# Kernel optimization log

Measured on AMD Instinct MI355X. Metric: run time of the kernel, lower is better.

Reference implementation:

```python
import jax, jax.numpy as jnp
import numpy as np

N = 100000      # nodes
E = 1600000     # edges (avg degree 16)
D_IN, D_HID, D_OUT = 128, 64, 32


def setup_inputs() -> dict:
    key = jax.random.key(0)
    ks = jax.random.split(key, 11)
    g = lambda k, shape, fan: jax.random.normal(k, shape, jnp.float32) * (1.0 / np.sqrt(fan))
    return {
        "x": jax.random.normal(ks[0], (N, D_IN), jnp.float32),
        "edges_index": jax.random.randint(ks[1], (2, E), 0, N, dtype=jnp.int64),
        # GATConv layer 1 (heads=1): linear weight, attention vectors a_src/a_dst, bias
        "W1": g(ks[2], (D_IN, D_HID), D_IN),
        "a_src1": g(ks[3], (D_HID,), D_HID),
        "a_dst1": g(ks[4], (D_HID,), D_HID),
        "b1": jnp.zeros((D_HID,), jnp.float32),
        # GATConv layer 2
        "W2": g(ks[5], (D_HID, D_OUT), D_HID),
        "a_src2": g(ks[6], (D_OUT,), D_OUT),
        "a_dst2": g(ks[7], (D_OUT,), D_OUT),
        "b2": jnp.zeros((D_OUT,), jnp.float32),
    }


def _gat_conv(x, src, dst, W, a_src, a_dst, b, n):
    """Single-head PyG GATConv: transform, edge attention, per-dst softmax, scatter-add."""
    h = x @ W                                        # [N, D]
    e = jax.nn.leaky_relu((h @ a_src)[src] + (h @ a_dst)[dst], 0.2)  # [E']
    # segment softmax over edges grouped by destination node
    m = jax.ops.segment_max(e, dst, num_segments=n)  # [N]
    w = jnp.exp(e - m[dst])                          # [E']
    s = jax.ops.segment_sum(w, dst, num_segments=n)  # [N]
    att = w / (s[dst] + 1e-16)                       # [E']
    out = jax.ops.segment_sum(att[:, None] * h[src], dst, num_segments=n)  # [N, D]
    return out + b


def reference(x, edges_index, W1, a_src1, a_dst1, b1, W2, a_src2, a_dst2, b2):
    n = x.shape[0]
    loops = jnp.arange(n, dtype=edges_index.dtype)   # GATConv add_self_loops=True
    src = jnp.concatenate([edges_index[0], loops])
    dst = jnp.concatenate([edges_index[1], loops])
    h = jax.nn.relu(_gat_conv(x, src, dst, W1, a_src1, a_dst1, b1, n))
    # F.dropout with training=False is identity (eval mode)
    out = _gat_conv(h, src, dst, W2, a_src2, a_dst2, b2, n)
    return jax.nn.log_softmax(out, axis=1)
```

## Files before the change

kernel.cpp:

```cpp
#include <hip/hip_runtime.h>
#include <math.h>

#define D_IN 128
#define D_HID 64
#define D_OUT 32
#define CAP 48
#define BSH 8
#define NB 391
#define CAPB 4608
#define CHUNK 8192
#define NPW 4
#define ESHIFT 5.0f
#define ECLAMP 16.0f

typedef __fp16 half2f __attribute__((ext_vector_type(2)));

__device__ __forceinline__ half2f u2h2(unsigned u) {
    union { unsigned u; half2f h; } c; c.u = u; return c.h;
}
__device__ __forceinline__ unsigned h22u(half2f h) {
    union { half2f h; unsigned u; } c; c.h = h; return c.u;
}
__device__ __forceinline__ unsigned short f2h(float f) {
    union { _Float16 h; unsigned short u; } c; c.h = (_Float16)f; return c.u;
}

#if defined(__has_builtin)
#  if __has_builtin(__builtin_amdgcn_fdot2)
#    define HAVE_FDOT2 1
#  else
#    define HAVE_FDOT2 0
#  endif
#else
#  define HAVE_FDOT2 0
#endif

__device__ __forceinline__ float fdot2f(half2f a, half2f b, float c) {
#if HAVE_FDOT2
    return __builtin_amdgcn_fdot2(a, b, c, false);
#else
    return fmaf((float)a.y, (float)b.y, fmaf((float)a.x, (float)b.x, c));
#endif
}

__device__ __forceinline__ void pair_acc(float wA, float wB, uint2 hA, uint2 hB,
                                         float& a0, float& a1, float& a2, float& a3)
{
    half2f wp = __builtin_amdgcn_cvt_pkrtz(wA, wB);
    a0 = fdot2f(wp, u2h2(__builtin_amdgcn_perm(hB.x, hA.x, 0x05040100u)), a0);
    a1 = fdot2f(wp, u2h2(__builtin_amdgcn_perm(hB.x, hA.x, 0x07060302u)), a1);
    a2 = fdot2f(wp, u2h2(__builtin_amdgcn_perm(hB.y, hA.y, 0x05040100u)), a2);
    a3 = fdot2f(wp, u2h2(__builtin_amdgcn_perm(hB.y, hA.y, 0x07060302u)), a3);
}


__global__ __launch_bounds__(256) void init_kernel(
    int* __restrict__ cnt, int* __restrict__ cursor, int n)
{
    int i = blockIdx.x * 256 + threadIdx.x;
    if (i < n) cnt[i] = 0;
    if (i < NB) cursor[i] = i * CAPB;
}

__global__ __launch_bounds__(256) void part_kernel(
    const int* __restrict__ esrc, const int* __restrict__ edst,
    unsigned long long* __restrict__ ebuf, int* __restrict__ cursor,
    int E, int Et)
{
    __shared__ int hist[NB];
    __shared__ int ofs[NB];
    const int t = threadIdx.x;
    const int base = blockIdx.x * CHUNK;
    const int end = min(base + CHUNK, Et);

    for (int b = t; b < NB; b += 256) hist[b] = 0;
    __syncthreads();
    for (int i = base + t; i < end; i += 256) {
        int d = (i < E) ? edst[i] : (i - E);
        atomicAdd(&hist[d >> BSH], 1);
    }
    __syncthreads();
    for (int b = t; b < NB; b += 256) {
        int c = hist[b];
        ofs[b] = c ? atomicAdd(&cursor[b], c) : 0;
    }
    __syncthreads();
    for (int i = base + t; i < end; i += 256) {
        int d = (i < E) ? edst[i] : (i - E);
        int s = (i < E) ? esrc[i] : (i - E);
        int p = atomicAdd(&ofs[d >> BSH], 1);
        ebuf[p] = ((unsigned long long)(unsigned)s << 32) | (unsigned)d;
    }
}

__global__ __launch_bounds__(256) void fill_bucket_kernel(
    const unsigned long long* __restrict__ ebuf, const int* __restrict__ cursor,
    int* __restrict__ cnt, int* __restrict__ csr_pad)
{
    int b = blockIdx.x;
    int beg = b * CAPB;
    int end = cursor[b];
    for (int i = beg + threadIdx.x; i < end; i += 256) {
        unsigned long long v = ebuf[i];
        int d = (int)(v & 0xffffffffu);
        int s = (int)(v >> 32);
        int slot = atomicAdd(&cnt[d], 1);
        if (slot < CAP) csr_pad[(size_t)d * CAP + slot] = s;
    }
}


template<int K, int NC, int RT, int PAD>
__global__ __launch_bounds__(256) void gemm_alpha_kernel(
    const float* __restrict__ A, const float* __restrict__ W,
    const float* __restrict__ a_src, const float* __restrict__ a_dst,
    unsigned short* __restrict__ C, float* __restrict__ as_,
    float* __restrict__ ad_, int M)
{
    constexpr int TM = 64;
    constexpr int CT = 4;
    constexpr int CG = NC / CT;
    constexpr int KS = K + PAD;
    __shared__ float xs[TM * KS];
    __shared__ float ws[K * NC];
    const int t = threadIdx.x;

    for (int i = t; i < K * NC / 4; i += 256)
        ((float4*)ws)[i] = ((const float4*)W)[i];

    const int base = blockIdx.x * TM;
    for (int i = t; i < TM * K / 4; i += 256) {
        int nloc = i / (K / 4);
        int k4   = i % (K / 4);
        int row  = base + nloc;
        float4 v = make_float4(0.f, 0.f, 0.f, 0.f);
        if (row < M)
            v = *(const float4*)(A + (size_t)row * K + k4 * 4);
        *(float4*)(xs + nloc * KS + k4 * 4) = v;
    }
    __syncthreads();

    const int tx = t % CG, ty = t / CG;
    const int r0 = ty * RT, c0 = tx * CT;
    float acc[RT][CT];
#pragma unroll
    for (int i = 0; i < RT; ++i)
#pragma unroll
        for (int j = 0; j < CT; ++j) acc[i][j] = 0.f;

    for (int k = 0; k < K; k += 4) {
        float4 a[RT];
#pragma unroll
        for (int i = 0; i < RT; ++i)
            a[i] = *(const float4*)(xs + (r0 + i) * KS + k);
#pragma unroll
        for (int kk = 0; kk < 4; ++kk) {
            float4 b = *(const float4*)(ws + (k + kk) * NC + c0);
#pragma unroll
            for (int i = 0; i < RT; ++i) {
                float av = kk == 0 ? a[i].x : kk == 1 ? a[i].y :
                           kk == 2 ? a[i].z : a[i].w;
                acc[i][0] = fmaf(av, b.x, acc[i][0]);
                acc[i][1] = fmaf(av, b.y, acc[i][1]);
                acc[i][2] = fmaf(av, b.z, acc[i][2]);
                acc[i][3] = fmaf(av, b.w, acc[i][3]);
            }
        }
    }

    const float4 asv = *(const float4*)(a_src + c0);
    const float4 adv = *(const float4*)(a_dst + c0);
#pragma unroll
    for (int i = 0; i < RT; ++i) {
        int row = base + r0 + i;
        float ps = acc[i][0] * asv.x + acc[i][1] * asv.y +
                   acc[i][2] * asv.z + acc[i][3] * asv.w;
        float pd = acc[i][0] * adv.x + acc[i][1] * adv.y +
                   acc[i][2] * adv.z + acc[i][3] * adv.w;
#pragma unroll
        for (int o = 1; o < CG; o <<= 1) {
            ps += __shfl_xor(ps, o);
            pd += __shfl_xor(pd, o);
        }
        if (row < M) {
            uint2 cv;
            cv.x = h22u(__builtin_amdgcn_cvt_pkrtz(acc[i][0], acc[i][1]));
            cv.y = h22u(__builtin_amdgcn_cvt_pkrtz(acc[i][2], acc[i][3]));
            *(uint2*)(C + (size_t)row * NC + c0) = cv;
            if (tx == 0) { as_[row] = ps; ad_[row] = pd; }
        }
    }
}

__global__ __launch_bounds__(256) void gat_aggr_fused_kernel(
    const int* __restrict__ cnt, const int* __restrict__ csr_pad,
    const float* __restrict__ as1, const float* __restrict__ ad1,
    const unsigned short* __restrict__ h1, const float* __restrict__ b1,
    const float* __restrict__ W2, const float* __restrict__ a2s,
    const float* __restrict__ a2d, unsigned short* __restrict__ h2,
    float* __restrict__ as2, float* __restrict__ ad2, int n)
{
    __shared__ float rbuf[4][64];
    const int t = threadIdx.x;
    const int wave = t >> 6;
    const int lane = t & 63;
    const int half = lane >> 5, j = lane & 31;

    float w2r[32];
#pragma unroll
    for (int k = 0; k < 32; ++k)
        w2r[k] = W2[(size_t)(half * 32 + k) * D_OUT + j];
    const float a2sj = a2s[j], a2dj = a2d[j];

    const int sub = lane >> 4;
    const int q4 = (lane & 15) * 4;
    const unsigned short* hq = h1 + q4;
    const float4 b1v = *(const float4*)(b1 + q4);

    const int d0 = (blockIdx.x * 4 + wave) * NPW;
    if (d0 >= n) return;

    for (int it = 0; it < NPW; ++it) {
        const int d = d0 + it;
        if (d >= n) break;

        const int   deg = min(cnt[d], CAP);
        const float add = ad1[d];
        int s = csr_pad[(size_t)d * CAP + lane];
        s = (lane < deg) ? s : 0;
        const float araw = as1[s];

        const int i0 = sub;
        int sA = __shfl(s, i0),      sB = __shfl(s, i0 + 4);
        int sC = __shfl(s, i0 + 8),  sD = __shfl(s, i0 + 12);
        uint2 hA = *(const uint2*)(hq + (size_t)sA * 64);
        uint2 hB = *(const uint2*)(hq + (size_t)sB * 64);
        uint2 hC = *(const uint2*)(hq + (size_t)sC * 64);
        uint2 hD = *(const uint2*)(hq + (size_t)sD * 64);
        const bool big = deg > 16;
        int sE = 0, sF = 0, sG = 0, sH = 0;
        uint2 hE, hF, hG, hH;
        if (big) {
            sE = __shfl(s, i0 + 16); sF = __shfl(s, i0 + 20);
            sG = __shfl(s, i0 + 24); sH = __shfl(s, i0 + 28);
            hE = *(const uint2*)(hq + (size_t)sE * 64);
            hF = *(const uint2*)(hq + (size_t)sF * 64);
            hG = *(const uint2*)(hq + (size_t)sG * 64);
            hH = *(const uint2*)(hq + (size_t)sH * 64);
        }

        float ev = araw + add;
        float e = (ev > 0.f) ? ev : 0.2f * ev;
        e = (lane < deg) ? fminf(e, ECLAMP) : -1e30f;
        float w = __expf(e - ESHIFT);
        float ssum = w;

        float a0 = 0.f, a1 = 0.f, a2v = 0.f, a3 = 0.f;
        {
            float wA = __shfl(w, i0),      wB = __shfl(w, i0 + 4);
            float wC = __shfl(w, i0 + 8),  wD = __shfl(w, i0 + 12);
            pair_acc(wA, wB, hA, hB, a0, a1, a2v, a3);
            pair_acc(wC, wD, hC, hD, a0, a1, a2v, a3);
            if (big) {
                float wE = __shfl(w, i0 + 16), wF = __shfl(w, i0 + 20);
                float wG = __shfl(w, i0 + 24), wH = __shfl(w, i0 + 28);
                pair_acc(wE, wF, hE, hF, a0, a1, a2v, a3);
                pair_acc(wG, wH, hG, hH, a0, a1, a2v, a3);
            }
        }
        if (deg > 32) {
            for (int tt = 32; tt < deg; tt += 16) {
                const int i1 = tt + sub;
                float wA = __shfl(w, i1),     wB = __shfl(w, i1 + 4);
                float wC = __shfl(w, i1 + 8), wD = __shfl(w, i1 + 12);
                int   tA = __shfl(s, i1),     tB = __shfl(s, i1 + 4);
                int   tC = __shfl(s, i1 + 8), tD = __shfl(s, i1 + 12);
                uint2 gA = *(const uint2*)(hq + (size_t)tA * 64);
                uint2 gB = *(const uint2*)(hq + (size_t)tB * 64);
                uint2 gC = *(const uint2*)(hq + (size_t)tC * 64);
                uint2 gD = *(const uint2*)(hq + (size_t)tD * 64);
                pair_acc(wA, wB, gA, gB, a0, a1, a2v, a3);
                pair_acc(wC, wD, gC, gD, a0, a1, a2v, a3);
            }
        }

#pragma unroll
        for (int o = 16; o <= 32; o <<= 1) {
            a0 += __shfl_xor(a0, o);  a1 += __shfl_xor(a1, o);
            a2v += __shfl_xor(a2v, o); a3 += __shfl_xor(a3, o);
        }
#pragma unroll
        for (int o = 32; o > 0; o >>= 1) ssum += __shfl_xor(ssum, o);

        const float inv = 1.0f / (ssum + 1e-16f);
        float4 rv;
        rv.x = fmaxf(fmaf(a0, inv, b1v.x), 0.f);
        rv.y = fmaxf(fmaf(a1, inv, b1v.y), 0.f);
        rv.z = fmaxf(fmaf(a2v, inv, b1v.z), 0.f);
        rv.w = fmaxf(fmaf(a3, inv, b1v.w), 0.f);
        if (sub == 0) *(float4*)(&rbuf[wave][q4]) = rv;

        const float* rb = &rbuf[wave][half * 32];
        float acc2 = 0.f;
#pragma unroll
        for (int k4 = 0; k4 < 8; ++k4) {
            float4 r4 = *(const float4*)(rb + k4 * 4);
            acc2 = fmaf(r4.x, w2r[k4 * 4 + 0], acc2);
            acc2 = fmaf(r4.y, w2r[k4 * 4 + 1], acc2);
            acc2 = fmaf(r4.z, w2r[k4 * 4 + 2], acc2);
            acc2 = fmaf(r4.w, w2r[k4 * 4 + 3], acc2);
        }
        acc2 += __shfl_xor(acc2, 32);

        float p1 = acc2 * a2sj, p2 = acc2 * a2dj;
#pragma unroll
        for (int o = 16; o > 0; o >>= 1) {
            p1 += __shfl_xor(p1, o);
            p2 += __shfl_xor(p2, o);
        }
        if (lane < 32) h2[(size_t)d * 32 + j] = f2h(acc2);
        if (lane == 0) { as2[d] = p1; ad2[d] = p2; }
    }
}

__global__ __launch_bounds__(256) void gat_aggr32_lsm_kernel(
    const int* __restrict__ cnt, const int* __restrict__ csr_pad,
    const float* __restrict__ as_, const float* __restrict__ ad_,
    const unsigned short* __restrict__ h, const float* __restrict__ bias,
    float* __restrict__ out, int n)
{
    const int wave = threadIdx.x >> 6;
    const int lane = threadIdx.x & 63;
    const int d0 = (blockIdx.x * 4 + wave) * NPW;
    if (d0 >= n) return;

    const int sub = lane >> 3;
    const int q4 = (lane & 7) * 4;
    const unsigned short* hq = h + q4;
    const float4 bv = *(const float4*)(bias + q4);

    for (int it = 0; it < NPW; ++it) {
        const int d = d0 + it;
        if (d >= n) break;

        const int   deg = min(cnt[d], CAP);
        const float add = ad_[d];
        int s = csr_pad[(size_t)d * CAP + lane];
        s = (lane < deg) ? s : 0;
        const float araw = as_[s];

        const int i0 = sub;
        int sA = __shfl(s, i0),      sB = __shfl(s, i0 + 8);
        uint2 hA = *(const uint2*)(hq + (size_t)sA * 32);
        uint2 hB = *(const uint2*)(hq + (size_t)sB * 32);
        const bool big = deg > 16;
        int sC = 0, sD = 0;
        uint2 hC, hD;
        if (big) {
            sC = __shfl(s, i0 + 16); sD = __shfl(s, i0 + 24);
            hC = *(const uint2*)(hq + (size_t)sC * 32);
            hD = *(const uint2*)(hq + (size_t)sD * 32);
        }

        float ev = araw + add;
        float e = (ev > 0.f) ? ev : 0.2f * ev;
        e = (lane < deg) ? fminf(e, ECLAMP) : -1e30f;
        float w = __expf(e - ESHIFT);
        float ssum = w;

        float a0 = 0.f, a1 = 0.f, a2v = 0.f, a3 = 0.f;
        {
            float wA = __shfl(w, i0), wB = __shfl(w, i0 + 8);
            pair_acc(wA, wB, hA, hB, a0, a1, a2v, a3);
            if (big) {
                float wC = __shfl(w, i0 + 16), wD = __shfl(w, i0 + 24);
                pair_acc(wC, wD, hC, hD, a0, a1, a2v, a3);
            }
        }
        if (deg > 32) {
            for (int tt = 32; tt < deg; tt += 16) {
                const int i1 = tt + sub;
                float wA = __shfl(w, i1); float wB = __shfl(w, i1 + 8);
                int   tA = __shfl(s, i1); int   tB = __shfl(s, i1 + 8);
                uint2 gA = *(const uint2*)(hq + (size_t)tA * 32);
                uint2 gB = *(const uint2*)(hq + (size_t)tB * 32);
                pair_acc(wA, wB, gA, gB, a0, a1, a2v, a3);
            }
        }
#pragma unroll
        for (int o = 8; o <= 32; o <<= 1) {
            a0 += __shfl_xor(a0, o);  a1 += __shfl_xor(a1, o);
            a2v += __shfl_xor(a2v, o); a3 += __shfl_xor(a3, o);
        }
#pragma unroll
        for (int o = 32; o > 0; o >>= 1) ssum += __shfl_xor(ssum, o);

        float inv = 1.0f / (ssum + 1e-16f);
        float r0 = fmaf(a0, inv, bv.x), r1 = fmaf(a1, inv, bv.y);
        float r2 = fmaf(a2v, inv, bv.z), r3 = fmaf(a3, inv, bv.w);

        float mx = fmaxf(fmaxf(r0, r1), fmaxf(r2, r3));
#pragma unroll
        for (int o = 1; o <= 4; o <<= 1) mx = fmaxf(mx, __shfl_xor(mx, o));
        float sm = __expf(r0 - mx) + __expf(r1 - mx) +
                   __expf(r2 - mx) + __expf(r3 - mx);
#pragma unroll
        for (int o = 1; o <= 4; o <<= 1) sm += __shfl_xor(sm, o);
        float lg = mx + __logf(sm);
        if (sub == 0) {
            float4 ov = make_float4(r0 - lg, r1 - lg, r2 - lg, r3 - lg);
            *(float4*)(out + (size_t)d * 32 + q4) = ov;
        }
    }
}

extern "C" void kernel_launch(void* const* d_in, const int* in_sizes, int n_in,
                              void* d_out, int out_size, void* d_ws, size_t ws_size,
                              hipStream_t stream) {
    const float* x    = (const float*)d_in[0];
    const int*   ei   = (const int*)  d_in[1];
    const float* W1   = (const float*)d_in[2];
    const float* av1s = (const float*)d_in[3];
    const float* av1d = (const float*)d_in[4];
    const float* b1   = (const float*)d_in[5];
    const float* W2   = (const float*)d_in[6];
    const float* av2s = (const float*)d_in[7];
    const float* av2d = (const float*)d_in[8];
    const float* b2   = (const float*)d_in[9];
    float* out = (float*)d_out;

    const int N  = in_sizes[0] / D_IN;
    const int E  = in_sizes[1] / 2;
    const int Et = E + N;
    const int* esrc = ei;
    const int* edst = ei + E;

    float* ws = (float*)d_ws;
    size_t off = 0;
    unsigned short* h1f = (unsigned short*)(ws + off); off += (size_t)N * 32;
    unsigned short* h2f_ = (unsigned short*)(ws + off); off += (size_t)N * 16;
    float* as1_ = ws + off;               off += N;
    float* ad1_ = ws + off;               off += N;
    float* as2_ = ws + off;               off += N;
    float* ad2_ = ws + off;               off += N;
    int* cnt    = (int*)(ws + off);       off += N;
    int* cursor = (int*)(ws + off);       off += NB + 1;
    int* csr_pad = (int*)(ws + off);      off += (size_t)N * CAP + 64;
    if (off & 1) off++;
    unsigned long long* ebuf = (unsigned long long*)(ws + off);
    off += (size_t)NB * CAPB * 2;

    const int tiles  = (N + 63) / 64;
    const int nblk   = (N + 255) / 256;
    const int aggblk = (N + 4 * NPW - 1) / (4 * NPW);
    const int pblk   = (Et + CHUNK - 1) / CHUNK;

    init_kernel<<<nblk, 256, 0, stream>>>(cnt, cursor, N);
    part_kernel<<<pblk, 256, 0, stream>>>(esrc, edst, ebuf, cursor, E, Et);
    fill_bucket_kernel<<<NB, 256, 0, stream>>>(ebuf, cursor, cnt, csr_pad);

    gemm_alpha_kernel<128, 64, 4, 0><<<tiles, 256, 0, stream>>>(
        x, W1, av1s, av1d, h1f, as1_, ad1_, N);

    gat_aggr_fused_kernel<<<aggblk, 256, 0, stream>>>(
        cnt, csr_pad, as1_, ad1_, h1f, b1,
        W2, av2s, av2d, h2f_, as2_, ad2_, N);

    gat_aggr32_lsm_kernel<<<aggblk, 256, 0, stream>>>(
        cnt, csr_pad, as2_, ad2_, h2f_, b2, out, N);
}
```

Measured before the change: 294.3 us.

## Replace two-pass bucketed edge partition with direct atomic scatter into padded CSR

```diff
diff --git a/kernel.cpp b/kernel.cpp
--- a/kernel.cpp
+++ b/kernel.cpp
@@ -5,10 +5,6 @@
 #define D_HID 64
 #define D_OUT 32
 #define CAP 48
-#define BSH 8
-#define NB 391
-#define CAPB 4608
-#define CHUNK 8192
 #define NPW 4
 #define ESHIFT 5.0f
 #define ECLAMP 16.0f
@@ -55,55 +51,20 @@
 
 
 __global__ __launch_bounds__(256) void init_kernel(
-    int* __restrict__ cnt, int* __restrict__ cursor, int n)
+    int* __restrict__ cnt, int n)
 {
     int i = blockIdx.x * 256 + threadIdx.x;
     if (i < n) cnt[i] = 0;
-    if (i < NB) cursor[i] = i * CAPB;
-}
-
-__global__ __launch_bounds__(256) void part_kernel(
+}
+
+__global__ __launch_bounds__(256) void scatter_kernel(
     const int* __restrict__ esrc, const int* __restrict__ edst,
-    unsigned long long* __restrict__ ebuf, int* __restrict__ cursor,
-    int E, int Et)
-{
-    __shared__ int hist[NB];
-    __shared__ int ofs[NB];
-    const int t = threadIdx.x;
-    const int base = blockIdx.x * CHUNK;
-    const int end = min(base + CHUNK, Et);
-
-    for (int b = t; b < NB; b += 256) hist[b] = 0;
-    __syncthreads();
-    for (int i = base + t; i < end; i += 256) {
-        int d = (i < E) ? edst[i] : (i - E);
-        atomicAdd(&hist[d >> BSH], 1);
-    }
-    __syncthreads();
-    for (int b = t; b < NB; b += 256) {
-        int c = hist[b];
-        ofs[b] = c ? atomicAdd(&cursor[b], c) : 0;
-    }
-    __syncthreads();
-    for (int i = base + t; i < end; i += 256) {
+    int* __restrict__ cnt, int* __restrict__ csr_pad, int E, int Et)
+{
+    const int stride = gridDim.x * 256;
+    for (int i = blockIdx.x * 256 + threadIdx.x; i < Et; i += stride) {
         int d = (i < E) ? edst[i] : (i - E);
         int s = (i < E) ? esrc[i] : (i - E);
-        int p = atomicAdd(&ofs[d >> BSH], 1);
-        ebuf[p] = ((unsigned long long)(unsigned)s << 32) | (unsigned)d;
-    }
-}
-
-__global__ __launch_bounds__(256) void fill_bucket_kernel(
-    const unsigned long long* __restrict__ ebuf, const int* __restrict__ cursor,
-    int* __restrict__ cnt, int* __restrict__ csr_pad)
-{
-    int b = blockIdx.x;
-    int beg = b * CAPB;
-    int end = cursor[b];
-    for (int i = beg + threadIdx.x; i < end; i += 256) {
-        unsigned long long v = ebuf[i];
-        int d = (int)(v & 0xffffffffu);
-        int s = (int)(v >> 32);
         int slot = atomicAdd(&cnt[d], 1);
         if (slot < CAP) csr_pad[(size_t)d * CAP + slot] = s;
     }
@@ -444,20 +405,15 @@
     float* as2_ = ws + off;               off += N;
     float* ad2_ = ws + off;               off += N;
     int* cnt    = (int*)(ws + off);       off += N;
-    int* cursor = (int*)(ws + off);       off += NB + 1;
     int* csr_pad = (int*)(ws + off);      off += (size_t)N * CAP + 64;
-    if (off & 1) off++;
-    unsigned long long* ebuf = (unsigned long long*)(ws + off);
-    off += (size_t)NB * CAPB * 2;
 
     const int tiles  = (N + 63) / 64;
     const int nblk   = (N + 255) / 256;
     const int aggblk = (N + 4 * NPW - 1) / (4 * NPW);
-    const int pblk   = (Et + CHUNK - 1) / CHUNK;
-
-    init_kernel<<<nblk, 256, 0, stream>>>(cnt, cursor, N);
-    part_kernel<<<pblk, 256, 0, stream>>>(esrc, edst, ebuf, cursor, E, Et);
-    fill_bucket_kernel<<<NB, 256, 0, stream>>>(ebuf, cursor, cnt, csr_pad);
+    const int sblk   = min((Et + 255) / 256, 2048);
+
+    init_kernel<<<nblk, 256, 0, stream>>>(cnt, N);
+    scatter_kernel<<<sblk, 256, 0, stream>>>(esrc, edst, cnt, csr_pad, E, Et);
 
     gemm_alpha_kernel<128, 64, 4, 0><<<tiles, 256, 0, stream>>>(
         x, W1, av1s, av1d, h1f, as1_, ad1_, N);
```

New measurement: 366.4 us. +24.5%, slower.

## Build padded CSR in shared memory per bucket with packed 32-bit edge keys

Applied to the files above, without the earlier changes.

```diff
diff --git a/kernel.cpp b/kernel.cpp
--- a/kernel.cpp
+++ b/kernel.cpp
@@ -8,7 +8,8 @@
 #define BSH 8
 #define NB 391
 #define CAPB 4608
-#define CHUNK 8192
+#define CHUNK 2048
+#define EPT (CHUNK / 256)
 #define NPW 4
 #define ESHIFT 5.0f
 #define ECLAMP 16.0f
@@ -54,30 +55,35 @@
 }
 
 
-__global__ __launch_bounds__(256) void init_kernel(
-    int* __restrict__ cnt, int* __restrict__ cursor, int n)
+__global__ __launch_bounds__(256) void init_kernel(int* __restrict__ cursor)
 {
     int i = blockIdx.x * 256 + threadIdx.x;
-    if (i < n) cnt[i] = 0;
     if (i < NB) cursor[i] = i * CAPB;
 }
 
 __global__ __launch_bounds__(256) void part_kernel(
     const int* __restrict__ esrc, const int* __restrict__ edst,
-    unsigned long long* __restrict__ ebuf, int* __restrict__ cursor,
-    int E, int Et)
+    unsigned* __restrict__ ebuf, int* __restrict__ cursor, int E, int Et)
 {
     __shared__ int hist[NB];
     __shared__ int ofs[NB];
     const int t = threadIdx.x;
     const int base = blockIdx.x * CHUNK;
-    const int end = min(base + CHUNK, Et);
 
     for (int b = t; b < NB; b += 256) hist[b] = 0;
     __syncthreads();
-    for (int i = base + t; i < end; i += 256) {
-        int d = (i < E) ? edst[i] : (i - E);
-        atomicAdd(&hist[d >> BSH], 1);
+
+    int dreg[EPT], sreg[EPT];
+#pragma unroll
+    for (int k = 0; k < EPT; ++k) {
+        int i = base + k * 256 + t;
+        int d = -1, s = 0;
+        if (i < Et) {
+            d = (i < E) ? edst[i] : (i - E);
+            s = (i < E) ? esrc[i] : (i - E);
+            atomicAdd(&hist[d >> BSH], 1);
+        }
+        dreg[k] = d; sreg[k] = s;
     }
     __syncthreads();
     for (int b = t; b < NB; b += 256) {
@@ -85,27 +91,62 @@
         ofs[b] = c ? atomicAdd(&cursor[b], c) : 0;
     }
     __syncthreads();
-    for (int i = base + t; i < end; i += 256) {
-        int d = (i < E) ? edst[i] : (i - E);
-        int s = (i < E) ? esrc[i] : (i - E);
-        int p = atomicAdd(&ofs[d >> BSH], 1);
-        ebuf[p] = ((unsigned long long)(unsigned)s << 32) | (unsigned)d;
+#pragma unroll
+    for (int k = 0; k < EPT; ++k) {
+        int d = dreg[k];
+        if (d >= 0) {
+            int bb = d >> BSH;
+            int p = atomicAdd(&ofs[bb], 1);
+            if (p < (bb + 1) * CAPB)
+                ebuf[p] = ((unsigned)sreg[k] << 8) | (unsigned)(d & 255);
+        }
     }
 }
 
 __global__ __launch_bounds__(256) void fill_bucket_kernel(
-    const unsigned long long* __restrict__ ebuf, const int* __restrict__ cursor,
-    int* __restrict__ cnt, int* __restrict__ csr_pad)
-{
-    int b = blockIdx.x;
-    int beg = b * CAPB;
-    int end = cursor[b];
-    for (int i = beg + threadIdx.x; i < end; i += 256) {
-        unsigned long long v = ebuf[i];
-        int d = (int)(v & 0xffffffffu);
-        int s = (int)(v >> 32);
-        int slot = atomicAdd(&cnt[d], 1);
-        if (slot < CAP) csr_pad[(size_t)d * CAP + slot] = s;
+    const unsigned* __restrict__ ebuf, const int* __restrict__ cursor,
+    int* __restrict__ cnt, int* __restrict__ csr_pad, int n)
+{
+    __shared__ __align__(16) int lrow[256 * CAP];
+    __shared__ int lcnt[256];
+    const int b = blockIdx.x;
+    const int t = threadIdx.x;
+    lcnt[t] = 0;
+    __syncthreads();
+
+    const int end = min(cursor[b], (b + 1) * CAPB);
+    for (int i = b * CAPB + t; i < end; i += 256) {
+        unsigned v = ebuf[i];
+        int dloc = (int)(v & 255u);
+        int s    = (int)(v >> 8);
+        int slot = atomicAdd(&lcnt[dloc], 1);
+        if (slot < CAP) lrow[dloc * CAP + slot] = s;
+    }
+    __syncthreads();
+
+    {
+        int m = min(lcnt[t], CAP);
+        int* row = lrow + t * CAP;
+        for (int a = 1; a < m; ++a) {
+            int key = row[a];
+            int p = a - 1;
+            while (p >= 0 && row[p] > key) { row[p + 1] = row[p]; --p; }
+            row[p + 1] = key;
+        }
+        for (int a = m; a < CAP; ++a) row[a] = 0;
+    }
+    __syncthreads();
+
+    const int node0 = b << BSH;
+    if (node0 + t < n) cnt[node0 + t] = lcnt[t];
+
+    int4* dst = (int4*)(csr_pad + (size_t)node0 * CAP);
+    const int4* src = (const int4*)lrow;
+    if (node0 + 256 <= n) {
+        for (int i = t; i < 256 * CAP / 4; i += 256) dst[i] = src[i];
+    } else {
+        const int lim = (n - node0) * CAP / 4;
+        for (int i = t; i < lim; i += 256) dst[i] = src[i];
     }
 }
 
@@ -444,20 +485,17 @@
     float* as2_ = ws + off;               off += N;
     float* ad2_ = ws + off;               off += N;
     int* cnt    = (int*)(ws + off);       off += N;
-    int* cursor = (int*)(ws + off);       off += NB + 1;
     int* csr_pad = (int*)(ws + off);      off += (size_t)N * CAP + 64;
-    if (off & 1) off++;
-    unsigned long long* ebuf = (unsigned long long*)(ws + off);
-    off += (size_t)NB * CAPB * 2;
+    int* cursor = (int*)(ws + off);       off += NB;
+    unsigned* ebuf = (unsigned*)(ws + off); off += (size_t)NB * CAPB;
 
     const int tiles  = (N + 63) / 64;
-    const int nblk   = (N + 255) / 256;
     const int aggblk = (N + 4 * NPW - 1) / (4 * NPW);
     const int pblk   = (Et + CHUNK - 1) / CHUNK;
 
-    init_kernel<<<nblk, 256, 0, stream>>>(cnt, cursor, N);
+    init_kernel<<<(NB + 255) / 256, 256, 0, stream>>>(cursor);
     part_kernel<<<pblk, 256, 0, stream>>>(esrc, edst, ebuf, cursor, E, Et);
-    fill_bucket_kernel<<<NB, 256, 0, stream>>>(ebuf, cursor, cnt, csr_pad);
+    fill_bucket_kernel<<<NB, 256, 0, stream>>>(ebuf, cursor, cnt, csr_pad, N);
 
     gemm_alpha_kernel<128, 64, 4, 0><<<tiles, 256, 0, stream>>>(
         x, W1, av1s, av1d, h1f, as1_, ad1_, N);
```

Result: slower. 319.7 us (+8.6%).
